# Kernel optimization log

Measured on AMD Instinct MI355X. Metric: run time of the kernel, lower is better.

## Reference

```python
import jax, jax.numpy as jnp
import numpy as np

D, H = 512, 1024

def setup_inputs() -> dict:
    key = jax.random.key(0)
    ks = jax.random.split(key, 7)
    s_ih = 1.0 / np.sqrt(H)
    return {
        "x": jax.random.normal(ks[0], (128, 512, D), dtype=jnp.float32),
        "W_ih": jax.random.uniform(ks[1], (4 * H, D), minval=-s_ih, maxval=s_ih, dtype=jnp.float32),
        "W_hh": jax.random.uniform(ks[2], (4 * H, H), minval=-s_ih, maxval=s_ih, dtype=jnp.float32),
        "b_ih": jax.random.uniform(ks[3], (4 * H,), minval=-s_ih, maxval=s_ih, dtype=jnp.float32),
        "b_hh": jax.random.uniform(ks[4], (4 * H,), minval=-s_ih, maxval=s_ih, dtype=jnp.float32),
        "fc_w": jax.random.uniform(ks[5], (H, H), minval=-s_ih, maxval=s_ih, dtype=jnp.float32),
        "fc_b": jax.random.uniform(ks[6], (H,), minval=-s_ih, maxval=s_ih, dtype=jnp.float32),
    }

def reference(x, W_ih, W_hh, b_ih, b_hh, fc_w, fc_b):
    # x: [batch, seq, d] -> time-major [seq, batch, d] (matches x.transpose(0,1))
    xt = jnp.swapaxes(x, 0, 1)
    n = x.shape[0]
    h = W_hh.shape[1]
    # Precompute input projections for all steps: [seq, batch, 4h]
    x_proj = jnp.einsum("tbd,gd->tbg", xt, W_ih) + b_ih + b_hh

    def step(carry, xp):
        hx, cx = carry
        gates = xp + hx @ W_hh.T  # [batch, 4h]
        i, f, g, o = jnp.split(gates, 4, axis=-1)  # PyTorch LSTMCell gate order
        i = jax.nn.sigmoid(i)
        f = jax.nn.sigmoid(f)
        g = jnp.tanh(g)
        o = jax.nn.sigmoid(o)
        cx = f * cx + i * g
        hx = o * jnp.tanh(cx)
        return (hx, cx), None

    h0 = jnp.zeros((n, h), dtype=x.dtype)
    c0 = jnp.zeros((n, h), dtype=x.dtype)
    (last_h, _), _ = jax.lax.scan(step, (h0, c0), x_proj)
    return last_h @ fc_w.T + fc_b
```

## Files before the change

### kernel.cpp

```cpp
#include <hip/hip_runtime.h>
#include <stdint.h>

#define BB   128
#define DD   512
#define HH   1024
#define SS   512
#define G4   4096
#define KKT  48
#define NT_FC 64
#define KK_FC 32
#define HSTEP 131072

typedef __attribute__((ext_vector_type(8))) short short8v;
typedef __attribute__((ext_vector_type(4))) float float4v;
typedef __attribute__((ext_vector_type(4))) unsigned int uint4v;

__device__ __forceinline__ unsigned short f2bf(float f) {
    union { float f; unsigned int u; } v; v.f = f;
    unsigned int u = v.u;
    unsigned int r = u + 0x7FFFu + ((u >> 16) & 1u);
    return (unsigned short)(r >> 16);
}
__device__ __forceinline__ float sigm(float z) { return 1.f / (1.f + __expf(-z)); }
__device__ __forceinline__ float tanh_f(float z) { float e = __expf(2.f * z); return 1.f - 2.f / (e + 1.f); }

__device__ __forceinline__ short8v cvt8(const float4 f0, const float4 f1) {
    short8v o;
    o[0]=(short)f2bf(f0.x); o[1]=(short)f2bf(f0.y); o[2]=(short)f2bf(f0.z); o[3]=(short)f2bf(f0.w);
    o[4]=(short)f2bf(f1.x); o[5]=(short)f2bf(f1.y); o[6]=(short)f2bf(f1.z); o[7]=(short)f2bf(f1.w);
    return o;
}

__global__ void pack_w_kernel(const float* __restrict__ W_ih,
                              const float* __restrict__ W_hh,
                              unsigned short* __restrict__ wp) {
    int idx = blockIdx.x * 256 + threadIdx.x;
    if (idx >= 256 * KKT * 64) return;
    int lane  = idx & 63;
    int kk    = (idx >> 6) % KKT;
    int ntile = idx / (64 * KKT);
    int q = ntile >> 6;
    int orow = q * HH + (ntile & 63) * 16 + (lane & 15);
    int kbase = kk * 32 + (lane >> 4) * 8;
    short8v ov;
#pragma unroll
    for (int i = 0; i < 8; ++i) {
        int k = kbase + i;
        float v = (k < DD) ? W_ih[(size_t)orow * DD + k]
                           : W_hh[(size_t)orow * HH + (k - DD)];
        ov[i] = (short)f2bf(v);
    }
    *(short8v*)&wp[(size_t)idx * 8] = ov;
}

__global__ void pack_fc_kernel(const float* __restrict__ fc_w,
                               unsigned short* __restrict__ wfc) {
    int idx = blockIdx.x * 256 + threadIdx.x;
    if (idx >= NT_FC * KK_FC * 64) return;
    int lane  = idx & 63;
    int kk    = (idx >> 6) % KK_FC;
    int ntile = idx / (64 * KK_FC);
    int o = ntile * 16 + (lane & 15);
    int kbase = kk * 32 + (lane >> 4) * 8;
    short8v ov;
#pragma unroll
    for (int i = 0; i < 8; ++i)
        ov[i] = (short)f2bf(fc_w[(size_t)o * HH + kbase + i]);
    *(short8v*)&wfc[(size_t)idx * 8] = ov;
}

__global__ void pack_x_kernel(const float* __restrict__ x,
                              unsigned short* __restrict__ xpre) {
    int idx = blockIdx.x * 256 + threadIdx.x;
    if (idx >= 8 * SS * 16 * 64) return;
    int lane  = idx & 63;
    int kk    = (idx >> 6) & 15;
    int t     = (idx >> 10) & (SS - 1);
    int mtile = idx >> 19;
    int b = mtile * 16 + (lane & 15);
    int d = kk * 32 + (lane >> 4) * 8;
    const float* src = &x[((size_t)b * SS + t) * DD + d];
    short8v ov;
#pragma unroll
    for (int i = 0; i < 8; ++i) ov[i] = (short)f2bf(src[i]);
    *(short8v*)&xpre[(size_t)idx * 8] = ov;
}

__global__ void init_kernel(const float* __restrict__ b_ih,
                            const float* __restrict__ b_hh,
                            unsigned short* __restrict__ h0,
                            float* __restrict__ bpp,
                            unsigned int* __restrict__ bar) {
    int i = blockIdx.x * 256 + threadIdx.x;
    if (i < BB * HH) h0[i] = 0;
    if (i < G4) { int j = i >> 2, q = i & 3; bpp[i] = b_ih[q * HH + j] + b_hh[q * HH + j]; }
    if (i < 4096) bar[i] = 0;
}

template<int PRE, int HIST>
__launch_bounds__(256, 2)
__global__ void lstm_persist(const float* __restrict__ x,
                             const unsigned short* __restrict__ xpre,
                             const unsigned short* __restrict__ wp,
                             const float* __restrict__ bp,
                             unsigned short* hh,
                             unsigned short* hbufB,
                             unsigned int* bar) {
    __shared__ __align__(16) unsigned short whl[4 * 12 * 64 * 8];
    __shared__ __align__(16) unsigned short hl[32 * 64 * 8];
    float* gl = (float*)hl;

    const int tid  = threadIdx.x;
    const int bid  = blockIdx.x;
    const int chain = bid >> 6;
    const int jg    = bid & 63;
    const int lane = tid & 63;
    const int w    = tid >> 6;
    const int l15  = lane & 15;
    const int lhi  = lane >> 4;

    const size_t ntb = (size_t)(w * 64 + jg) * KKT;
    short8v wx[16];
#pragma unroll
    for (int kk = 0; kk < 16; ++kk)
        wx[kk] = *(const short8v*)&wp[((ntb + kk) * 64 + lane) * 8];
#pragma unroll
    for (int kk = 0; kk < 16; ++kk)
        asm volatile("" : "+v"(wx[kk]));

#pragma unroll
    for (int i = 0; i < 12; ++i) {
        int f  = tid + 256 * i;
        int ln = f & 63, kkl = (f >> 6) % 12, wq = (f >> 6) / 12;
        *(short8v*)&whl[(size_t)f * 8] =
            *(const short8v*)&wp[(((size_t)(wq * 64 + jg) * KKT + 16 + kkl) * 64 + ln) * 8];
    }

    const int erow = (tid & 127) >> 3;
    const int eup  = (tid & 7) * 2;
    const float4 eb0 = *(const float4*)&bp[(jg * 16 + eup) * 4];
    const float4 eb1 = *(const float4*)&bp[(jg * 16 + eup + 1) * 4];
    float ec0 = 0.f, ec1 = 0.f;
    const int ekkh = jg >> 1;
    const int esub = (jg & 1) * 2 + (eup >> 3);
    const size_t esoff = ((size_t)(chain * 32 + ekkh) * 64 + (esub * 16 + erow)) * 8 + (eup & 7);

    __syncthreads();

    if (chain >= 4) {
#pragma unroll 1
        for (int i = 0; i < 6; ++i) __builtin_amdgcn_s_sleep(15);
    }

#pragma unroll 1
    for (int t = 0; t < SS; ++t) {
        const unsigned short* hin;
        unsigned short* hout;
        if (HIST) {
            hin  = hh + (size_t)t * HSTEP;
            hout = hh + (size_t)(t + 1) * HSTEP;
        } else {
            hin  = (t & 1) ? hbufB : hh;
            hout = (t & 1) ? hh : hbufB;
        }

        __syncthreads();

        if (t > 0 && tid == 0)
            __hip_atomic_store(&bar[chain * 64 + jg], (unsigned int)t,
                               __ATOMIC_RELAXED, __HIP_MEMORY_SCOPE_AGENT);

        float4v acce = {0.f, 0.f, 0.f, 0.f};
        float4v acco = {0.f, 0.f, 0.f, 0.f};

#pragma unroll
        for (int kk = 0; kk < 16; kk += 2) {
            short8v a0, a1;
            if (PRE) {
                a0 = *(const short8v*)&xpre[(((size_t)(chain * SS + t) * 16 + kk) * 64 + lane) * 8];
                a1 = *(const short8v*)&xpre[(((size_t)(chain * SS + t) * 16 + kk + 1) * 64 + lane) * 8];
            } else {
                const float* p0 = &x[((size_t)(chain * 16 + l15) * SS + t) * DD + kk * 32 + lhi * 8];
                a0 = cvt8(*(const float4*)p0, *(const float4*)(p0 + 4));
                a1 = cvt8(*(const float4*)(p0 + 32), *(const float4*)(p0 + 36));
            }
            acce = __builtin_amdgcn_mfma_f32_16x16x32_bf16(a0, wx[kk], acce, 0, 0, 0);
            acco = __builtin_amdgcn_mfma_f32_16x16x32_bf16(a1, wx[kk + 1], acco, 0, 0, 0);
        }

        if (t > 0 && w == 0) {
            const unsigned int tgt = (unsigned int)t;
            for (;;) {
                unsigned int v = __hip_atomic_load(&bar[chain * 64 + lane],
                                                   __ATOMIC_RELAXED, __HIP_MEMORY_SCOPE_AGENT);
                if (!__any(v < tgt)) break;
                __builtin_amdgcn_s_sleep(1);
            }
        }
        __syncthreads();

        {
            const char* hsrc = (const char*)hin + (size_t)chain * 32768 + (size_t)tid * 16;
            char* ldst = (char*)hl + (size_t)tid * 16;
            if (HIST) {
                uint4v r0 = *(const uint4v*)(hsrc);
                uint4v r1 = *(const uint4v*)(hsrc + 4096);
                uint4v r2 = *(const uint4v*)(hsrc + 8192);
                uint4v r3 = *(const uint4v*)(hsrc + 12288);
                uint4v r4 = *(const uint4v*)(hsrc + 16384);
                uint4v r5 = *(const uint4v*)(hsrc + 20480);
                uint4v r6 = *(const uint4v*)(hsrc + 24576);
                uint4v r7 = *(const uint4v*)(hsrc + 28672);
                *(uint4v*)(ldst)         = r0;
                *(uint4v*)(ldst + 4096)  = r1;
                *(uint4v*)(ldst + 8192)  = r2;
                *(uint4v*)(ldst + 12288) = r3;
                *(uint4v*)(ldst + 16384) = r4;
                *(uint4v*)(ldst + 20480) = r5;
                *(uint4v*)(ldst + 24576) = r6;
                *(uint4v*)(ldst + 28672) = r7;
            } else {
                uint4v r0,r1,r2,r3,r4,r5,r6,r7;
                asm volatile("global_load_dwordx4 %0, %1, off sc0 sc1" : "=v"(r0) : "v"(hsrc));
                asm volatile("global_load_dwordx4 %0, %1, off sc0 sc1" : "=v"(r1) : "v"(hsrc + 4096));
                asm volatile("global_load_dwordx4 %0, %1, off sc0 sc1" : "=v"(r2) : "v"(hsrc + 8192));
                asm volatile("global_load_dwordx4 %0, %1, off sc0 sc1" : "=v"(r3) : "v"(hsrc + 12288));
                asm volatile("global_load_dwordx4 %0, %1, off sc0 sc1" : "=v"(r4) : "v"(hsrc + 16384));
                asm volatile("global_load_dwordx4 %0, %1, off sc0 sc1" : "=v"(r5) : "v"(hsrc + 20480));
                asm volatile("global_load_dwordx4 %0, %1, off sc0 sc1" : "=v"(r6) : "v"(hsrc + 24576));
                asm volatile("global_load_dwordx4 %0, %1, off sc0 sc1" : "=v"(r7) : "v"(hsrc + 28672));
                asm volatile("s_waitcnt vmcnt(0)" ::: "memory");
                __builtin_amdgcn_sched_barrier(0);
                *(uint4v*)(ldst)         = r0;
                *(uint4v*)(ldst + 4096)  = r1;
                *(uint4v*)(ldst + 8192)  = r2;
                *(uint4v*)(ldst + 12288) = r3;
                *(uint4v*)(ldst + 16384) = r4;
                *(uint4v*)(ldst + 20480) = r5;
                *(uint4v*)(ldst + 24576) = r6;
                *(uint4v*)(ldst + 28672) = r7;
            }
        }
        __syncthreads();

#pragma unroll
        for (int kkh = 0; kkh < 32; kkh += 2) {
            short8v a0 = *(const short8v*)((char*)hl + kkh * 1024 + lane * 16);
            short8v a1 = *(const short8v*)((char*)hl + (kkh + 1) * 1024 + lane * 16);
            short8v b0, b1;
            if (kkh < 12) b0 = *(const short8v*)&whl[(size_t)((w * 12 + kkh) * 64 + lane) * 8];
            else          b0 = *(const short8v*)&wp[((ntb + 16 + kkh) * 64 + lane) * 8];
            if (kkh + 1 < 12) b1 = *(const short8v*)&whl[(size_t)((w * 12 + kkh + 1) * 64 + lane) * 8];
            else              b1 = *(const short8v*)&wp[((ntb + 16 + kkh + 1) * 64 + lane) * 8];
            acce = __builtin_amdgcn_mfma_f32_16x16x32_bf16(a0, b0, acce, 0, 0, 0);
            acco = __builtin_amdgcn_mfma_f32_16x16x32_bf16(a1, b1, acco, 0, 0, 0);
        }
        __syncthreads();

#pragma unroll
        for (int r = 0; r < 4; ++r)
            gl[(lhi * 4 + r) * 68 + l15 * 4 + w] = acce[r] + acco[r];
        __syncthreads();

        if (tid < 128) {
            float4 g0 = *(const float4*)&gl[erow * 68 + (eup + 0) * 4];
            float4 g1 = *(const float4*)&gl[erow * 68 + (eup + 1) * 4];
            float h0v, h1v;
            {
                float ig = sigm(g0.x + eb0.x), fg = sigm(g0.y + eb0.y);
                float gg = tanh_f(g0.z + eb0.z), og = sigm(g0.w + eb0.w);
                ec0 = fg * ec0 + ig * gg; h0v = og * tanh_f(ec0);
            }
            {
                float ig = sigm(g1.x + eb1.x), fg = sigm(g1.y + eb1.y);
                float gg = tanh_f(g1.z + eb1.z), og = sigm(g1.w + eb1.w);
                ec1 = fg * ec1 + ig * gg; h1v = og * tanh_f(ec1);
            }
            unsigned int hv = (unsigned int)f2bf(h0v) | ((unsigned int)f2bf(h1v) << 16);
            const unsigned short* hp = hout + esoff;
            asm volatile("global_store_dword %0, %1, off sc0 sc1"
                         :: "v"(hp), "v"(hv) : "memory");
        }
        asm volatile("s_waitcnt vmcnt(0)" ::: "memory");
    }
}

__launch_bounds__(256)
__global__ void fc_kernel(const unsigned short* __restrict__ hfin,
                          const unsigned short* __restrict__ wfc,
                          const float* __restrict__ fc_b,
                          float* __restrict__ out) {
    const int tid = threadIdx.x, bid = blockIdx.x;
    const int mg = bid >> 4;
    const int ng = bid & 15;
    const int lane = tid & 63, wave = tid >> 6;
    const int wm = wave >> 1, wn = wave & 1;

    float4v acc[2][2] = {};
#pragma unroll
    for (int kkg = 0; kkg < 32; ++kkg) {
        short8v a[2], b[2];
#pragma unroll
        for (int mtl = 0; mtl < 2; ++mtl) {
            int gm = mg * 4 + wm * 2 + mtl;
            a[mtl] = *(const short8v*)&hfin[((size_t)(gm * 32 + kkg) * 64 + lane) * 8];
        }
#pragma unroll
        for (int nt = 0; nt < 2; ++nt) {
            int ntile = ng * 4 + wn * 2 + nt;
            b[nt] = *(const short8v*)&wfc[(((size_t)ntile * KK_FC + kkg) * 64 + lane) * 8];
        }
#pragma unroll
        for (int mtl = 0; mtl < 2; ++mtl)
#pragma unroll
            for (int nt = 0; nt < 2; ++nt)
                acc[mtl][nt] = __builtin_amdgcn_mfma_f32_16x16x32_bf16(
                    a[mtl], b[nt], acc[mtl][nt], 0, 0, 0);
    }
#pragma unroll
    for (int mtl = 0; mtl < 2; ++mtl)
#pragma unroll
        for (int nt = 0; nt < 2; ++nt)
#pragma unroll
            for (int r = 0; r < 4; ++r) {
                int mrow = mg * 64 + wm * 32 + mtl * 16 + (lane >> 4) * 4 + r;
                int o = ng * 64 + wn * 32 + nt * 16 + (lane & 15);
                out[(size_t)mrow * HH + o] = acc[mtl][nt][r] + fc_b[o];
            }
}

extern "C" void kernel_launch(void* const* d_in, const int* in_sizes, int n_in,
                              void* d_out, int out_size, void* d_ws, size_t ws_size,
                              hipStream_t stream) {
    const float* x    = (const float*)d_in[0];
    const float* W_ih = (const float*)d_in[1];
    const float* W_hh = (const float*)d_in[2];
    const float* b_ih = (const float*)d_in[3];
    const float* b_hh = (const float*)d_in[4];
    const float* fc_w = (const float*)d_in[5];
    const float* fc_b = (const float*)d_in[6];
    float* out = (float*)d_out;

    char* ws = (char*)d_ws;
    size_t off = 0;
    unsigned short* wp  = (unsigned short*)(ws + off); off += (size_t)256 * KKT * 64 * 8 * 2;
    unsigned short* wfc = (unsigned short*)(ws + off); off += (size_t)NT_FC * KK_FC * 64 * 8 * 2;
    float* bp  = (float*)(ws + off); off += (size_t)G4 * 4;
    unsigned int* bar = (unsigned int*)(ws + off); off += 4096 * 4;
    unsigned short* hbase = (unsigned short*)(ws + off);
    size_t hist_bytes = (size_t)(SS + 1) * HSTEP * 2;
    size_t pp_bytes   = (size_t)2 * HSTEP * 2;
    size_t xpre_bytes = (size_t)8 * SS * 16 * 64 * 8 * 2;

    const bool hist = (ws_size >= off + hist_bytes);
    size_t hb = hist ? hist_bytes : pp_bytes;
    if (ws_size < off + hb) return;
    unsigned short* xpre = (unsigned short*)(ws + off + hb);
    const bool pre = (ws_size >= off + hb + xpre_bytes);

    unsigned short* hbufB = hist ? (unsigned short*)nullptr : (hbase + HSTEP);

    pack_w_kernel<<<3072, 256, 0, stream>>>(W_ih, W_hh, wp);
    pack_fc_kernel<<<512, 256, 0, stream>>>(fc_w, wfc);
    init_kernel<<<512, 256, 0, stream>>>(b_ih, b_hh, hbase, bp, bar);
    if (pre) pack_x_kernel<<<16384, 256, 0, stream>>>(x, xpre);

    if (hist) {
        if (pre) lstm_persist<1,1><<<512, 256, 0, stream>>>(x, xpre, wp, bp, hbase, hbufB, bar);
        else     lstm_persist<0,1><<<512, 256, 0, stream>>>(x, xpre, wp, bp, hbase, hbufB, bar);
    } else {
        if (pre) lstm_persist<1,0><<<512, 256, 0, stream>>>(x, xpre, wp, bp, hbase, hbufB, bar);
        else     lstm_persist<0,0><<<512, 256, 0, stream>>>(x, xpre, wp, bp, hbase, hbufB, bar);
    }

    const unsigned short* hfin = hist ? (hbase + (size_t)SS * HSTEP) : hbase;
    fc_kernel<<<32, 256, 0, stream>>>(hfin, wfc, fc_b, out);
}
```

Before: 2.024 ms.

## Process two batch chains per persistent block, halving grid to one block per CU

Each persistent block now owns two independent batch chains (cA and cB = cA+4) instead of one, so the grid drops from 512 to 256 blocks with launch bounds of one block per CU. The recurrent step for chain B is interleaved after chain A's elementwise update, so A's global h store and barrier signal can overlap with the wait, h load and MFMA work for chain B. The gate scratch buffer moves to its own shared array so it no longer aliases the h tile. The trade-off is serialized per-step work inside each block and the loss of the second co-resident block per CU, which previously hid latency, plus doubled per-block register state.

```diff
diff --git a/kernel.cpp b/kernel.cpp
--- a/kernel.cpp
+++ b/kernel.cpp
@@ -10,6 +10,7 @@
 #define NT_FC 64
 #define KK_FC 32
 #define HSTEP 131072
+#define WLK  12
 
 typedef __attribute__((ext_vector_type(8))) short short8v;
 typedef __attribute__((ext_vector_type(4))) float float4v;
@@ -98,7 +99,7 @@
 }
 
 template<int PRE, int HIST>
-__launch_bounds__(256, 2)
+__launch_bounds__(256, 1)
 __global__ void lstm_persist(const float* __restrict__ x,
                              const unsigned short* __restrict__ xpre,
                              const unsigned short* __restrict__ wp,
@@ -106,14 +107,16 @@
                              unsigned short* hh,
                              unsigned short* hbufB,
                              unsigned int* bar) {
-    __shared__ __align__(16) unsigned short whl[4 * 12 * 64 * 8];
+    __shared__ __align__(16) unsigned short whl[4 * WLK * 64 * 8];
     __shared__ __align__(16) unsigned short hl[32 * 64 * 8];
-    float* gl = (float*)hl;
+    __shared__ __align__(16) float gl[16 * 68 + 4];
 
     const int tid  = threadIdx.x;
     const int bid  = blockIdx.x;
-    const int chain = bid >> 6;
-    const int jg    = bid & 63;
+    const int pr   = bid >> 6;
+    const int jg   = bid & 63;
+    const int cA   = pr;
+    const int cB   = pr + 4;
     const int lane = tid & 63;
     const int w    = tid >> 6;
     const int l15  = lane & 15;
@@ -129,9 +132,9 @@
         asm volatile("" : "+v"(wx[kk]));
 
 #pragma unroll
-    for (int i = 0; i < 12; ++i) {
+    for (int i = 0; i < WLK; ++i) {
         int f  = tid + 256 * i;
-        int ln = f & 63, kkl = (f >> 6) % 12, wq = (f >> 6) / 12;
+        int ln = f & 63, kkl = (f >> 6) % WLK, wq = (f >> 6) / WLK;
         *(short8v*)&whl[(size_t)f * 8] =
             *(const short8v*)&wp[(((size_t)(wq * 64 + jg) * KKT + 16 + kkl) * 64 + ln) * 8];
     }
@@ -140,58 +143,72 @@
     const int eup  = (tid & 7) * 2;
     const float4 eb0 = *(const float4*)&bp[(jg * 16 + eup) * 4];
     const float4 eb1 = *(const float4*)&bp[(jg * 16 + eup + 1) * 4];
-    float ec0 = 0.f, ec1 = 0.f;
+    float ecA0 = 0.f, ecA1 = 0.f, ecB0 = 0.f, ecB1 = 0.f;
     const int ekkh = jg >> 1;
     const int esub = (jg & 1) * 2 + (eup >> 3);
-    const size_t esoff = ((size_t)(chain * 32 + ekkh) * 64 + (esub * 16 + erow)) * 8 + (eup & 7);
+    const size_t esbase = ((size_t)ekkh * 64 + (esub * 16 + erow)) * 8 + (eup & 7);
+    const size_t esoffA = (size_t)cA * 32 * 512 + esbase;
+    const size_t esoffB = (size_t)cB * 32 * 512 + esbase;
 
     __syncthreads();
-
-    if (chain >= 4) {
-#pragma unroll 1
-        for (int i = 0; i < 6; ++i) __builtin_amdgcn_s_sleep(15);
-    }
 
 #pragma unroll 1
     for (int t = 0; t < SS; ++t) {
-        const unsigned short* hin;
-        unsigned short* hout;
+        const unsigned short *hinA, *hinB;
+        unsigned short *houtA, *houtB;
         if (HIST) {
-            hin  = hh + (size_t)t * HSTEP;
-            hout = hh + (size_t)(t + 1) * HSTEP;
+            hinA  = hh + (size_t)t * HSTEP;       houtA = hh + (size_t)(t + 1) * HSTEP;
+            hinB  = hinA;                          houtB = houtA;
         } else {
-            hin  = (t & 1) ? hbufB : hh;
-            hout = (t & 1) ? hh : hbufB;
-        }
-
-        __syncthreads();
-
-        if (t > 0 && tid == 0)
-            __hip_atomic_store(&bar[chain * 64 + jg], (unsigned int)t,
+            hinA  = (t & 1) ? hbufB : hh;          houtA = (t & 1) ? hh : hbufB;
+            hinB  = hinA;                          houtB = houtA;
+        }
+
+        asm volatile("s_waitcnt vmcnt(0)" ::: "memory");
+        __syncthreads();
+        if (t > 0 && tid == 0) {
+            __hip_atomic_store(&bar[cA * 64 + jg], (unsigned int)t,
                                __ATOMIC_RELAXED, __HIP_MEMORY_SCOPE_AGENT);
-
-        float4v acce = {0.f, 0.f, 0.f, 0.f};
-        float4v acco = {0.f, 0.f, 0.f, 0.f};
+            __hip_atomic_store(&bar[cB * 64 + jg], (unsigned int)t,
+                               __ATOMIC_RELAXED, __HIP_MEMORY_SCOPE_AGENT);
+        }
+
+        float4v aAe = {0.f,0.f,0.f,0.f}, aAo = {0.f,0.f,0.f,0.f};
+        float4v aBe = {0.f,0.f,0.f,0.f}, aBo = {0.f,0.f,0.f,0.f};
 
 #pragma unroll
         for (int kk = 0; kk < 16; kk += 2) {
             short8v a0, a1;
             if (PRE) {
-                a0 = *(const short8v*)&xpre[(((size_t)(chain * SS + t) * 16 + kk) * 64 + lane) * 8];
-                a1 = *(const short8v*)&xpre[(((size_t)(chain * SS + t) * 16 + kk + 1) * 64 + lane) * 8];
+                a0 = *(const short8v*)&xpre[(((size_t)(cA * SS + t) * 16 + kk) * 64 + lane) * 8];
+                a1 = *(const short8v*)&xpre[(((size_t)(cA * SS + t) * 16 + kk + 1) * 64 + lane) * 8];
             } else {
-                const float* p0 = &x[((size_t)(chain * 16 + l15) * SS + t) * DD + kk * 32 + lhi * 8];
+                const float* p0 = &x[((size_t)(cA * 16 + l15) * SS + t) * DD + kk * 32 + lhi * 8];
                 a0 = cvt8(*(const float4*)p0, *(const float4*)(p0 + 4));
                 a1 = cvt8(*(const float4*)(p0 + 32), *(const float4*)(p0 + 36));
             }
-            acce = __builtin_amdgcn_mfma_f32_16x16x32_bf16(a0, wx[kk], acce, 0, 0, 0);
-            acco = __builtin_amdgcn_mfma_f32_16x16x32_bf16(a1, wx[kk + 1], acco, 0, 0, 0);
+            aAe = __builtin_amdgcn_mfma_f32_16x16x32_bf16(a0, wx[kk], aAe, 0, 0, 0);
+            aAo = __builtin_amdgcn_mfma_f32_16x16x32_bf16(a1, wx[kk + 1], aAo, 0, 0, 0);
+        }
+#pragma unroll
+        for (int kk = 0; kk < 16; kk += 2) {
+            short8v a0, a1;
+            if (PRE) {
+                a0 = *(const short8v*)&xpre[(((size_t)(cB * SS + t) * 16 + kk) * 64 + lane) * 8];
+                a1 = *(const short8v*)&xpre[(((size_t)(cB * SS + t) * 16 + kk + 1) * 64 + lane) * 8];
+            } else {
+                const float* p0 = &x[((size_t)(cB * 16 + l15) * SS + t) * DD + kk * 32 + lhi * 8];
+                a0 = cvt8(*(const float4*)p0, *(const float4*)(p0 + 4));
+                a1 = cvt8(*(const float4*)(p0 + 32), *(const float4*)(p0 + 36));
+            }
+            aBe = __builtin_amdgcn_mfma_f32_16x16x32_bf16(a0, wx[kk], aBe, 0, 0, 0);
+            aBo = __builtin_amdgcn_mfma_f32_16x16x32_bf16(a1, wx[kk + 1], aBo, 0, 0, 0);
         }
 
         if (t > 0 && w == 0) {
             const unsigned int tgt = (unsigned int)t;
             for (;;) {
-                unsigned int v = __hip_atomic_load(&bar[chain * 64 + lane],
+                unsigned int v = __hip_atomic_load(&bar[cA * 64 + lane],
                                                    __ATOMIC_RELAXED, __HIP_MEMORY_SCOPE_AGENT);
                 if (!__any(v < tgt)) break;
                 __builtin_amdgcn_s_sleep(1);
@@ -200,7 +217,7 @@
         __syncthreads();
 
         {
-            const char* hsrc = (const char*)hin + (size_t)chain * 32768 + (size_t)tid * 16;
+            const char* hsrc = (const char*)hinA + (size_t)cA * 32768 + (size_t)tid * 16;
             char* ldst = (char*)hl + (size_t)tid * 16;
             if (HIST) {
                 uint4v r0 = *(const uint4v*)(hsrc);
@@ -211,14 +228,10 @@
                 uint4v r5 = *(const uint4v*)(hsrc + 20480);
                 uint4v r6 = *(const uint4v*)(hsrc + 24576);
                 uint4v r7 = *(const uint4v*)(hsrc + 28672);
-                *(uint4v*)(ldst)         = r0;
-                *(uint4v*)(ldst + 4096)  = r1;
-                *(uint4v*)(ldst + 8192)  = r2;
-                *(uint4v*)(ldst + 12288) = r3;
-                *(uint4v*)(ldst + 16384) = r4;
-                *(uint4v*)(ldst + 20480) = r5;
-                *(uint4v*)(ldst + 24576) = r6;
-                *(uint4v*)(ldst + 28672) = r7;
+                *(uint4v*)(ldst)         = r0; *(uint4v*)(ldst + 4096)  = r1;
+                *(uint4v*)(ldst + 8192)  = r2; *(uint4v*)(ldst + 12288) = r3;
+                *(uint4v*)(ldst + 16384) = r4; *(uint4v*)(ldst + 20480) = r5;
+                *(uint4v*)(ldst + 24576) = r6; *(uint4v*)(ldst + 28672) = r7;
             } else {
                 uint4v r0,r1,r2,r3,r4,r5,r6,r7;
                 asm volatile("global_load_dwordx4 %0, %1, off sc0 sc1" : "=v"(r0) : "v"(hsrc));
@@ -231,14 +244,10 @@
                 asm volatile("global_load_dwordx4 %0, %1, off sc0 sc1" : "=v"(r7) : "v"(hsrc + 28672));
                 asm volatile("s_waitcnt vmcnt(0)" ::: "memory");
                 __builtin_amdgcn_sched_barrier(0);
-                *(uint4v*)(ldst)         = r0;
-                *(uint4v*)(ldst + 4096)  = r1;
-                *(uint4v*)(ldst + 8192)  = r2;
-                *(uint4v*)(ldst + 12288) = r3;
-                *(uint4v*)(ldst + 16384) = r4;
-                *(uint4v*)(ldst + 20480) = r5;
-                *(uint4v*)(ldst + 24576) = r6;
-                *(uint4v*)(ldst + 28672) = r7;
+                *(uint4v*)(ldst)         = r0; *(uint4v*)(ldst + 4096)  = r1;
+                *(uint4v*)(ldst + 8192)  = r2; *(uint4v*)(ldst + 12288) = r3;
+                *(uint4v*)(ldst + 16384) = r4; *(uint4v*)(ldst + 20480) = r5;
+                *(uint4v*)(ldst + 24576) = r6; *(uint4v*)(ldst + 28672) = r7;
             }
         }
         __syncthreads();
@@ -248,18 +257,17 @@
             short8v a0 = *(const short8v*)((char*)hl + kkh * 1024 + lane * 16);
             short8v a1 = *(const short8v*)((char*)hl + (kkh + 1) * 1024 + lane * 16);
             short8v b0, b1;
-            if (kkh < 12) b0 = *(const short8v*)&whl[(size_t)((w * 12 + kkh) * 64 + lane) * 8];
-            else          b0 = *(const short8v*)&wp[((ntb + 16 + kkh) * 64 + lane) * 8];
-            if (kkh + 1 < 12) b1 = *(const short8v*)&whl[(size_t)((w * 12 + kkh + 1) * 64 + lane) * 8];
-            else              b1 = *(const short8v*)&wp[((ntb + 16 + kkh + 1) * 64 + lane) * 8];
-            acce = __builtin_amdgcn_mfma_f32_16x16x32_bf16(a0, b0, acce, 0, 0, 0);
-            acco = __builtin_amdgcn_mfma_f32_16x16x32_bf16(a1, b1, acco, 0, 0, 0);
-        }
-        __syncthreads();
+            if (kkh < WLK) b0 = *(const short8v*)&whl[(size_t)((w * WLK + kkh) * 64 + lane) * 8];
+            else           b0 = *(const short8v*)&wp[((ntb + 16 + kkh) * 64 + lane) * 8];
+            if (kkh + 1 < WLK) b1 = *(const short8v*)&whl[(size_t)((w * WLK + kkh + 1) * 64 + lane) * 8];
+            else               b1 = *(const short8v*)&wp[((ntb + 16 + kkh + 1) * 64 + lane) * 8];
+            aAe = __builtin_amdgcn_mfma_f32_16x16x32_bf16(a0, b0, aAe, 0, 0, 0);
+            aAo = __builtin_amdgcn_mfma_f32_16x16x32_bf16(a1, b1, aAo, 0, 0, 0);
+        }
 
 #pragma unroll
         for (int r = 0; r < 4; ++r)
-            gl[(lhi * 4 + r) * 68 + l15 * 4 + w] = acce[r] + acco[r];
+            gl[(lhi * 4 + r) * 68 + l15 * 4 + w] = aAe[r] + aAo[r];
         __syncthreads();
 
         if (tid < 128) {
@@ -269,20 +277,106 @@
             {
                 float ig = sigm(g0.x + eb0.x), fg = sigm(g0.y + eb0.y);
                 float gg = tanh_f(g0.z + eb0.z), og = sigm(g0.w + eb0.w);
-                ec0 = fg * ec0 + ig * gg; h0v = og * tanh_f(ec0);
+                ecA0 = fg * ecA0 + ig * gg; h0v = og * tanh_f(ecA0);
             }
             {
                 float ig = sigm(g1.x + eb1.x), fg = sigm(g1.y + eb1.y);
                 float gg = tanh_f(g1.z + eb1.z), og = sigm(g1.w + eb1.w);
-                ec1 = fg * ec1 + ig * gg; h1v = og * tanh_f(ec1);
+                ecA1 = fg * ecA1 + ig * gg; h1v = og * tanh_f(ecA1);
             }
             unsigned int hv = (unsigned int)f2bf(h0v) | ((unsigned int)f2bf(h1v) << 16);
-            const unsigned short* hp = hout + esoff;
+            const unsigned short* hp = houtA + esoffA;
             asm volatile("global_store_dword %0, %1, off sc0 sc1"
                          :: "v"(hp), "v"(hv) : "memory");
         }
-        asm volatile("s_waitcnt vmcnt(0)" ::: "memory");
+
+        if (t > 0 && w == 0) {
+            const unsigned int tgt = (unsigned int)t;
+            for (;;) {
+                unsigned int v = __hip_atomic_load(&bar[cB * 64 + lane],
+                                                   __ATOMIC_RELAXED, __HIP_MEMORY_SCOPE_AGENT);
+                if (!__any(v < tgt)) break;
+                __builtin_amdgcn_s_sleep(1);
+            }
+        }
+        __syncthreads();
+
+        {
+            const char* hsrc = (const char*)hinB + (size_t)cB * 32768 + (size_t)tid * 16;
+            char* ldst = (char*)hl + (size_t)tid * 16;
+            if (HIST) {
+                uint4v r0 = *(const uint4v*)(hsrc);
+                uint4v r1 = *(const uint4v*)(hsrc + 4096);
+                uint4v r2 = *(const uint4v*)(hsrc + 8192);
+                uint4v r3 = *(const uint4v*)(hsrc + 12288);
+                uint4v r4 = *(const uint4v*)(hsrc + 16384);
+                uint4v r5 = *(const uint4v*)(hsrc + 20480);
+                uint4v r6 = *(const uint4v*)(hsrc + 24576);
+                uint4v r7 = *(const uint4v*)(hsrc + 28672);
+                *(uint4v*)(ldst)         = r0; *(uint4v*)(ldst + 4096)  = r1;
+                *(uint4v*)(ldst + 8192)  = r2; *(uint4v*)(ldst + 12288) = r3;
+                *(uint4v*)(ldst + 16384) = r4; *(uint4v*)(ldst + 20480) = r5;
+                *(uint4v*)(ldst + 24576) = r6; *(uint4v*)(ldst + 28672) = r7;
+            } else {
+                uint4v r0,r1,r2,r3,r4,r5,r6,r7;
+                asm volatile("global_load_dwordx4 %0, %1, off sc0 sc1" : "=v"(r0) : "v"(hsrc));
+                asm volatile("global_load_dwordx4 %0, %1, off sc0 sc1" : "=v"(r1) : "v"(hsrc + 4096));
+                asm volatile("global_load_dwordx4 %0, %1, off sc0 sc1" : "=v"(r2) : "v"(hsrc + 8192));
+                asm volatile("global_load_dwordx4 %0, %1, off sc0 sc1" : "=v"(r3) : "v"(hsrc + 12288));
+                asm volatile("global_load_dwordx4 %0, %1, off sc0 sc1" : "=v"(r4) : "v"(hsrc + 16384));
+                asm volatile("global_load_dwordx4 %0, %1, off sc0 sc1" : "=v"(r5) : "v"(hsrc + 20480));
+                asm volatile("global_load_dwordx4 %0, %1, off sc0 sc1" : "=v"(r6) : "v"(hsrc + 24576));
+                asm volatile("global_load_dwordx4 %0, %1, off sc0 sc1" : "=v"(r7) : "v"(hsrc + 28672));
+                asm volatile("s_waitcnt vmcnt(0)" ::: "memory");
+                __builtin_amdgcn_sched_barrier(0);
+                *(uint4v*)(ldst)         = r0; *(uint4v*)(ldst + 4096)  = r1;
+                *(uint4v*)(ldst + 8192)  = r2; *(uint4v*)(ldst + 12288) = r3;
+                *(uint4v*)(ldst + 16384) = r4; *(uint4v*)(ldst + 20480) = r5;
+                *(uint4v*)(ldst + 24576) = r6; *(uint4v*)(ldst + 28672) = r7;
+            }
+        }
+        __syncthreads();
+
+#pragma unroll
+        for (int kkh = 0; kkh < 32; kkh += 2) {
+            short8v a0 = *(const short8v*)((char*)hl + kkh * 1024 + lane * 16);
+            short8v a1 = *(const short8v*)((char*)hl + (kkh + 1) * 1024 + lane * 16);
+            short8v b0, b1;
+            if (kkh < WLK) b0 = *(const short8v*)&whl[(size_t)((w * WLK + kkh) * 64 + lane) * 8];
+            else           b0 = *(const short8v*)&wp[((ntb + 16 + kkh) * 64 + lane) * 8];
+            if (kkh + 1 < WLK) b1 = *(const short8v*)&whl[(size_t)((w * WLK + kkh + 1) * 64 + lane) * 8];
+            else               b1 = *(const short8v*)&wp[((ntb + 16 + kkh + 1) * 64 + lane) * 8];
+            aBe = __builtin_amdgcn_mfma_f32_16x16x32_bf16(a0, b0, aBe, 0, 0, 0);
+            aBo = __builtin_amdgcn_mfma_f32_16x16x32_bf16(a1, b1, aBo, 0, 0, 0);
+        }
+        __syncthreads();
+
+#pragma unroll
+        for (int r = 0; r < 4; ++r)
+            gl[(lhi * 4 + r) * 68 + l15 * 4 + w] = aBe[r] + aBo[r];
+        __syncthreads();
+
+        if (tid < 128) {
+            float4 g0 = *(const float4*)&gl[erow * 68 + (eup + 0) * 4];
+            float4 g1 = *(const float4*)&gl[erow * 68 + (eup + 1) * 4];
+            float h0v, h1v;
+            {
+                float ig = sigm(g0.x + eb0.x), fg = sigm(g0.y + eb0.y);
+                float gg = tanh_f(g0.z + eb0.z), og = sigm(g0.w + eb0.w);
+                ecB0 = fg * ecB0 + ig * gg; h0v = og * tanh_f(ecB0);
+            }
+            {
+                float ig = sigm(g1.x + eb1.x), fg = sigm(g1.y + eb1.y);
+                float gg = tanh_f(g1.z + eb1.z), og = sigm(g1.w + eb1.w);
+                ecB1 = fg * ecB1 + ig * gg; h1v = og * tanh_f(ecB1);
+            }
+            unsigned int hv = (unsigned int)f2bf(h0v) | ((unsigned int)f2bf(h1v) << 16);
+            const unsigned short* hp = houtB + esoffB;
+            asm volatile("global_store_dword %0, %1, off sc0 sc1"
+                         :: "v"(hp), "v"(hv) : "memory");
+        }
     }
+    asm volatile("s_waitcnt vmcnt(0)" ::: "memory");
 }
 
 __launch_bounds__(256)
@@ -366,11 +460,11 @@
     if (pre) pack_x_kernel<<<16384, 256, 0, stream>>>(x, xpre);
 
     if (hist) {
-        if (pre) lstm_persist<1,1><<<512, 256, 0, stream>>>(x, xpre, wp, bp, hbase, hbufB, bar);
-        else     lstm_persist<0,1><<<512, 256, 0, stream>>>(x, xpre, wp, bp, hbase, hbufB, bar);
+        if (pre) lstm_persist<1,1><<<256, 256, 0, stream>>>(x, xpre, wp, bp, hbase, hbufB, bar);
+        else     lstm_persist<0,1><<<256, 256, 0, stream>>>(x, xpre, wp, bp, hbase, hbufB, bar);
     } else {
-        if (pre) lstm_persist<1,0><<<512, 256, 0, stream>>>(x, xpre, wp, bp, hbase, hbufB, bar);
-        else     lstm_persist<0,0><<<512, 256, 0, stream>>>(x, xpre, wp, bp, hbase, hbufB, bar);
+        if (pre) lstm_persist<1,0><<<256, 256, 0, stream>>>(x, xpre, wp, bp, hbase, hbufB, bar);
+        else     lstm_persist<0,0><<<256, 256, 0, stream>>>(x, xpre, wp, bp, hbase, hbufB, bar);
     }
 
     const unsigned short* hfin = hist ? (hbase + (size_t)SS * HSTEP) : hbase;
```

Result: slower. 3.463 ms (+71.1%).
